# Kernel optimization log

Hardware: AMD Instinct MI355X
Metric: run time of the kernel (lower is better)

Reference implementation:

```python
import jax, jax.numpy as jnp
import numpy as np

# SLAYER SRM-ALPHA neuron / simulation constants (from netParams)
THETA = 10.0      # spike threshold
TAU_SR = 10.0     # PSP (SRM) time constant
TAU_REF = 1.0     # refractory time constant
SCALE_REF = 2.0
TAU_RHO = 1.0     # surrogate-gradient width (unused in fwd)
SCALE_RHO = 1.0
TS = 1.0
K_SRM = 100       # truncation of alpha kernel (values < 1e-4 beyond this)
K_REF = 16

def _alpha_kernel(tau, K, mult):
    t = jnp.arange(K, dtype=jnp.float32) * TS
    return mult * (t / tau) * jnp.exp(1.0 - t / tau)

SRM_KERNEL = _alpha_kernel(TAU_SR, K_SRM, 1.0)                       # eps(t)
REF_KERNEL = _alpha_kernel(TAU_REF, K_REF, -2.0 * THETA * SCALE_REF)  # nu(t)

def heaviside(u):
    return (u >= THETA).astype(u.dtype)

def psp(x):
    # causal temporal convolution with SRM alpha kernel; x: (..., T)
    T = x.shape[-1]
    K = SRM_KERNEL.shape[0]
    flat = x.reshape(-1, 1, T)  # (N, C=1, T)
    out = jax.lax.conv_general_dilated(flat, SRM_KERNEL[::-1].reshape(1, 1, K),
                                       (1,), [(K - 1, 0)])
    return out.reshape(x.shape)

def spike(v):
    # SLAYER spike generation with refractory feedback; v: (..., T)
    refk = REF_KERNEL[1:]          # refractory affects strictly future steps
    L = refk.shape[0]
    vT = jnp.moveaxis(v, -1, 0)    # (T, ...)
    pend0 = jnp.zeros(vT.shape[1:] + (L,), v.dtype)  # pending refractory contributions
    def step(pend, vt):
        u = vt + pend[..., 0]
        s = heaviside(u)
        pend = jnp.concatenate([pend[..., 1:], jnp.zeros_like(pend[..., :1])], axis=-1) \
               + s[..., None] * refk
        return pend, s
    _, sT = jax.lax.scan(step, pend0, vT)
    return jnp.moveaxis(sT, 0, -1)

def conv_t(x, W, pad):
    # per-timestep 2D conv (slayer.conv uses Conv3d with kernel (k,k,1), no bias)
    B, C, H, Wd, T = x.shape
    xt = jnp.transpose(x, (0, 4, 1, 2, 3)).reshape(B * T, C, H, Wd)
    y = jax.lax.conv_general_dilated(xt, W, (1, 1), [(pad, pad), (pad, pad)])
    Co, Ho, Wo = y.shape[1:]
    return jnp.transpose(y.reshape(B, T, Co, Ho, Wo), (0, 2, 3, 4, 1))

def pool_t(x):
    # slayer.pool(2): 2x2 sum-pool with constant weight 1.1*theta per element
    s = jax.lax.reduce_window(x, 0.0, jax.lax.add, (1, 1, 2, 2, 1), (1, 1, 2, 2, 1), 'VALID')
    return s * (1.1 * THETA)

def _forward(spikeInput, W1, W2, W3, W4, Wfc):
    x = spike(conv_t(psp(spikeInput), W1, 1))   # (B,16,48,48,T)
    x = spike(pool_t(psp(x)))                   # (B,16,24,24,T)
    x = spike(conv_t(psp(x), W2, 1))            # (B,32,24,24,T)
    x = spike(pool_t(psp(x)))                   # (B,32,12,12,T)
    x = spike(conv_t(psp(x), W3, 1))            # (B,64,12,12,T)
    x = spike(pool_t(psp(x)))                   # (B,64,6,6,T)
    x = spike(conv_t(psp(x), W4, 1))            # (B,64,6,6,T)
    x = spike(jnp.einsum('bchwt,kchw->bkt', psp(x), Wfc))  # (B,10,T)
    return x

def setup_inputs():
    key = jax.random.key(0)
    ks = jax.random.split(key, 6)
    B, T = 4, 200
    spikeInput = (jax.random.uniform(ks[0], (B, 2, 50, 50, T)) < 0.05).astype(jnp.float32)
    W1 = 0.5 * jax.random.normal(ks[1], (16, 2, 5, 5), jnp.float32)
    W2 = 0.25 * jax.random.normal(ks[2], (32, 16, 3, 3), jnp.float32)
    W3 = 0.25 * jax.random.normal(ks[3], (64, 32, 3, 3), jnp.float32)
    W4 = 0.25 * jax.random.normal(ks[4], (64, 64, 3, 3), jnp.float32)
    Wfc = 0.1 * jax.random.normal(ks[5], (10, 64, 6, 6), jnp.float32)
    return {"spikeInput": spikeInput, "W1": W1, "W2": W2, "W3": W3, "W4": W4, "Wfc": Wfc}

def reference(spikeInput, W1, W2, W3, W4, Wfc):
    return _forward(spikeInput, W1, W2, W3, W4, Wfc)
```

## Files before the change

kernel.cpp:

```cpp
#include <hip/hip_runtime.h>
#include <math.h>


#define THETA 10.0f
#define RSTRIDE 204

__global__ void prep_kernel(const float* __restrict__ W1, const float* __restrict__ W2,
                            const float* __restrict__ W3, const float* __restrict__ W4,
                            float* HQ, float* rk,
                            float* wt1, float* wt2, float* wt3, float* wt4) {
    int i = blockIdx.x * 256 + threadIdx.x;
    if (i < 144) {
        int k = i - 15;
        float val = 0.0f;
        if (k >= 0 && k <= 99) {
            float tf = (float)k;
            float x = tf / 10.0f;
            val = x * (float)exp((double)(1.0f - x));
        }
        HQ[i] = val;
    } else if (i < 160) {
        int j = i - 144;
        if (j < 15) {
            float t = (float)(j + 1);
            rk[j] = (-40.0f * t) * (float)exp((double)(1.0f - t));
        }
    } else if (i < 960) {
        int j = i - 160, co = j / 50, tp = j % 50;
        wt1[tp * 16 + co] = W1[j];
    } else if (i < 5568) {
        int j = i - 960, co = j / 144, tp = j % 144;
        wt2[tp * 32 + co] = W2[j];
    } else if (i < 24000) {
        int j = i - 5568, co = j / 288, tp = j % 288;
        wt3[tp * 64 + co] = W3[j];
    } else if (i < 60864) {
        int j = i - 24000, co = j / 576, tp = j % 576;
        wt4[tp * 64 + co] = W4[j];
    }
}

#define FIR_STEP(A0, A1, A2, A3, qx, qy, qz, qw, hA, hB)  \
    A0 = fmaf(hA.x, qw, A0);                              \
    A1 = fmaf(hA.y, qw, A1);                              \
    A2 = fmaf(hA.z, qw, A2);                              \
    A3 = fmaf(hA.w, qw, A3);                              \
    A0 = fmaf(hA.y, qz, A0);                              \
    A1 = fmaf(hA.z, qz, A1);                              \
    A2 = fmaf(hA.w, qz, A2);                              \
    A3 = fmaf(hB.x, qz, A3);                              \
    A0 = fmaf(hA.z, qy, A0);                              \
    A1 = fmaf(hA.w, qy, A1);                              \
    A2 = fmaf(hB.x, qy, A2);                              \
    A3 = fmaf(hB.y, qy, A3);                              \
    A0 = fmaf(hA.w, qx, A0);                              \
    A1 = fmaf(hB.x, qx, A1);                              \
    A2 = fmaf(hB.y, qx, A2);                              \
    A3 = fmaf(hB.z, qx, A3);

#define SCAN4(XV, p, rk)                                          \
    {                                                             \
        float u_, sv_;                                            \
        u_ = XV.x + p[0]; sv_ = (u_ >= THETA) ? 1.0f : 0.0f;      \
        XV.x = sv_;                                               \
        _Pragma("unroll")                                         \
        for (int i_ = 0; i_ < 14; ++i_) p[i_] = fmaf(sv_, rk[i_], p[i_ + 1]); \
        p[14] = sv_ * rk[14];                                     \
        u_ = XV.y + p[0]; sv_ = (u_ >= THETA) ? 1.0f : 0.0f;      \
        XV.y = sv_;                                               \
        _Pragma("unroll")                                         \
        for (int i_ = 0; i_ < 14; ++i_) p[i_] = fmaf(sv_, rk[i_], p[i_ + 1]); \
        p[14] = sv_ * rk[14];                                     \
        u_ = XV.z + p[0]; sv_ = (u_ >= THETA) ? 1.0f : 0.0f;      \
        XV.z = sv_;                                               \
        _Pragma("unroll")                                         \
        for (int i_ = 0; i_ < 14; ++i_) p[i_] = fmaf(sv_, rk[i_], p[i_ + 1]); \
        p[14] = sv_ * rk[14];                                     \
        u_ = XV.w + p[0]; sv_ = (u_ >= THETA) ? 1.0f : 0.0f;      \
        XV.w = sv_;                                               \
        _Pragma("unroll")                                         \
        for (int i_ = 0; i_ < 14; ++i_) p[i_] = fmaf(sv_, rk[i_], p[i_ + 1]); \
        p[14] = sv_ * rk[14];                                     \
    }

__device__ __forceinline__ void fir_run2(const float* __restrict__ row,
                                         const float4* __restrict__ HQ4,
                                         int t0, int jend, float4 (&acc)[2]) {
    float4 A = HQ4[2], B = HQ4[3], C = HQ4[4];
    const float* bp = row + t0 + 4;
    for (int j = 0; j <= jend; ++j) {
        const float4 qv = *reinterpret_cast<const float4*>(bp);
        const float4 N = HQ4[j + 5];
        FIR_STEP(acc[0].x, acc[0].y, acc[0].z, acc[0].w,
                 qv.x, qv.y, qv.z, qv.w, A, B)
        FIR_STEP(acc[1].x, acc[1].y, acc[1].z, acc[1].w,
                 qv.x, qv.y, qv.z, qv.w, B, C)
        A = B; B = C; C = N;
        bp -= 4;
    }
}

__device__ static const signed char FIR_ITEMS8[8][4] = {
    {24, 12, 8, -1}, {22, 21, 4, -1}, {20, 19, 3, -1}, {18, 17, 2, -1},
    {16, 15, 1, 0},  {13, 11, 5, -1}, {14, 10, 6, -1}, {23, 9, 7, -1}};

template <bool SCAN>
__global__ __launch_bounds__(512) void spikepsp_kernel(const float* __restrict__ in,
                                                       float* __restrict__ out,
                                                       const float* __restrict__ HQ,
                                                       const float* __restrict__ rkt,
                                                       int n) {
    __shared__ __align__(16) float tile[64 * RSTRIDE];
    const int l = threadIdx.x & 63;
    const int w = threadIdx.x >> 6;
    const int s0 = blockIdx.x * 64;
    for (int i = threadIdx.x; i < 3200; i += 512) {
        const int slot = i / 50, q = i - slot * 50;
        const int ser = s0 + slot;
        float4 v = make_float4(0.f, 0.f, 0.f, 0.f);
        if (ser < n) v = *reinterpret_cast<const float4*>(in + (long)ser * 200 + 4 * q);
        *reinterpret_cast<float4*>(&tile[slot * RSTRIDE + 4 * q]) = v;
    }
    __syncthreads();
    if (SCAN) {
        if (w == 0) {
            float rk[15];
            #pragma unroll
            for (int i = 0; i < 15; ++i) rk[i] = rkt[i];
            float p[15];
            #pragma unroll
            for (int i = 0; i < 15; ++i) p[i] = 0.0f;
            float* row = tile + l * RSTRIDE;
            for (int tq = 0; tq < 50; ++tq) {
                float4 xv = *reinterpret_cast<const float4*>(&row[4 * tq]);
                SCAN4(xv, p, rk)
                *reinterpret_cast<float4*>(&row[4 * tq]) = xv;
            }
        }
        __syncthreads();
    }
    const bool valid = (s0 + l) < n;
    const float* row = tile + l * RSTRIDE;
    const float4* HQ4 = reinterpret_cast<const float4*>(HQ);
    float* op = out + (long)(s0 + l) * 200;
    #pragma unroll
    for (int k = 0; k < 4; ++k) {
        const int id = FIR_ITEMS8[w][k];
        if (id < 0) break;
        const int t0 = 8 * id;
        const int jend = ((2 * id < 25) ? 2 * id : 25) + 1;
        float4 acc[2];
        acc[0] = make_float4(0.f, 0.f, 0.f, 0.f);
        acc[1] = make_float4(0.f, 0.f, 0.f, 0.f);
        fir_run2(row, HQ4, t0, jend, acc);
        if (valid) {
            *reinterpret_cast<float4*>(op + t0) = acc[0];
            *reinterpret_cast<float4*>(op + t0 + 4) = acc[1];
        }
    }
}

__global__ __launch_bounds__(512) void spikepsppool_kernel(const float* __restrict__ in,
                                                           float* __restrict__ out,
                                                           const float* __restrict__ HQ,
                                                           const float* __restrict__ rkt,
                                                           int C, int HO, int WO) {
    __shared__ __align__(16) float tile[64 * RSTRIDE];
    __shared__ int sbase[64];
    const int l = threadIdx.x & 63;
    const int w = threadIdx.x >> 6;
    const int o0 = blockIdx.x * 16;
    const int H = 2 * HO, W = 2 * WO;
    if (threadIdx.x < 64) {
        const int oi = threadIdx.x >> 2, p = threadIdx.x & 3;
        const int o = o0 + oi;
        const int wo = o % WO; int tmp = o / WO;
        const int ho = tmp % HO; tmp /= HO;
        const int c = tmp % C; const int b = tmp / C;
        sbase[threadIdx.x] = ((b * C + c) * H + 2 * ho + (p >> 1)) * W + 2 * wo + (p & 1);
    }
    __syncthreads();
    for (int i = threadIdx.x; i < 3200; i += 512) {
        const int slot = i / 50, q = i - slot * 50;
        const float4 v = *reinterpret_cast<const float4*>(in + (long)sbase[slot] * 200 + 4 * q);
        *reinterpret_cast<float4*>(&tile[slot * RSTRIDE + 4 * q]) = v;
    }
    __syncthreads();
    if (w == 0) {
        float rk[15];
        #pragma unroll
        for (int i = 0; i < 15; ++i) rk[i] = rkt[i];
        float p[15];
        #pragma unroll
        for (int i = 0; i < 15; ++i) p[i] = 0.0f;
        float* row = tile + l * RSTRIDE;
        for (int tq = 0; tq < 50; ++tq) {
            float4 xv = *reinterpret_cast<const float4*>(&row[4 * tq]);
            SCAN4(xv, p, rk)
            *reinterpret_cast<float4*>(&row[4 * tq]) = xv;
        }
    }
    __syncthreads();
    const int qb = l & ~3;
    const float* row = tile + l * RSTRIDE;
    const float4* HQ4 = reinterpret_cast<const float4*>(HQ);
    float* op = out + (long)(o0 + (l >> 2)) * 200;
    auto qsum = [&](float v) -> float {
        const float v0 = __shfl(v, qb + 0);
        const float v1 = __shfl(v, qb + 1);
        const float v2 = __shfl(v, qb + 2);
        const float v3 = __shfl(v, qb + 3);
        return (((v0 + v1) + v2) + v3) * 11.0f;
    };
    #pragma unroll
    for (int k = 0; k < 4; ++k) {
        const int id = FIR_ITEMS8[w][k];
        if (id < 0) break;
        const int t0 = 8 * id;
        const int jend = ((2 * id < 25) ? 2 * id : 25) + 1;
        float4 acc[2];
        acc[0] = make_float4(0.f, 0.f, 0.f, 0.f);
        acc[1] = make_float4(0.f, 0.f, 0.f, 0.f);
        fir_run2(row, HQ4, t0, jend, acc);
        #pragma unroll
        for (int d = 0; d < 2; ++d) {
            float4 r;
            r.x = qsum(acc[d].x); r.y = qsum(acc[d].y);
            r.z = qsum(acc[d].z); r.w = qsum(acc[d].w);
            if ((l & 3) == 0)
                *reinterpret_cast<float4*>(op + t0 + 4 * d) = r;
        }
    }
}

template <int K, int PAD, int CI, int COG>
__global__ __launch_bounds__(256) void conv_kernel(const float* __restrict__ x,
                                                   const float* __restrict__ wt,
                                                   float* __restrict__ out,
                                                   int Co, int H, int W,
                                                   int HO, int WO) {
    const int l = threadIdx.x & 63;
    const int wv = threadIdx.x >> 6;
    if (l >= 50) return;
    const int p = blockIdx.x * 4 + wv;
    const int wo = p % WO, ho = p / WO;
    const int co0 = blockIdx.y * COG;
    const int b = blockIdx.z;
    const int t0 = l * 4;
    float4 acc[COG];
    #pragma unroll
    for (int c = 0; c < COG; ++c) acc[c] = make_float4(0.f, 0.f, 0.f, 0.f);
    const float* xb = x + ((long)b * CI * H * W) * 200 + t0;
    for (int ci = 0; ci < CI; ++ci) {
        #pragma unroll
        for (int kh = 0; kh < K; ++kh) {
            const int hi = ho + kh - PAD;
            if (hi < 0 || hi >= H) continue;
            #pragma unroll
            for (int kw = 0; kw < K; ++kw) {
                const int wi = wo + kw - PAD;
                if (wi < 0 || wi >= W) continue;
                const float4 v = *reinterpret_cast<const float4*>(
                    xb + ((long)(ci * H + hi) * W + wi) * 200);
                const float* wp = wt + ((ci * K + kh) * K + kw) * Co + co0;
                #pragma unroll
                for (int c = 0; c < COG; ++c) {
                    const float wv_ = wp[c];
                    acc[c].x = fmaf(wv_, v.x, acc[c].x);
                    acc[c].y = fmaf(wv_, v.y, acc[c].y);
                    acc[c].z = fmaf(wv_, v.z, acc[c].z);
                    acc[c].w = fmaf(wv_, v.w, acc[c].w);
                }
            }
        }
    }
    const long hwN = (long)HO * WO;
    const long ob = ((long)(b * Co + co0) * HO + ho) * WO + wo;
    #pragma unroll
    for (int c = 0; c < COG; ++c)
        *reinterpret_cast<float4*>(out + (ob + c * hwN) * 200 + t0) = acc[c];
}

template <int CI, int COG>
__global__ __launch_bounds__(256) void conv3_kernel(const float* __restrict__ x,
                                                    const float* __restrict__ wt,
                                                    float* __restrict__ out,
                                                    int Co, int H, int W) {
    const int l = threadIdx.x & 63;
    const int wv = threadIdx.x >> 6;
    if (l >= 50) return;
    const int p = blockIdx.x * 4 + wv;
    const int wo = p % W, ho = p / W;
    const int co0 = blockIdx.y * COG;
    const int b = blockIdx.z;
    const int t0 = l * 4;
    float4 acc[COG];
    #pragma unroll
    for (int c = 0; c < COG; ++c) acc[c] = make_float4(0.f, 0.f, 0.f, 0.f);

    bool vm[9];
    #pragma unroll
    for (int i = 0; i < 9; ++i) {
        const int hi = ho + i / 3 - 1, wi = wo + i % 3 - 1;
        vm[i] = (hi >= 0) && (hi < H) && (wi >= 0) && (wi < W);
    }
    const long cis = (long)H * W * 200;
    const float* pb = x + (long)b * CI * cis + ((long)(ho - 1) * W + (wo - 1)) * 200 + t0;

    float4 bufA[9], bufB[9];
    auto ld = [&](int ci, float4 (&B)[9]) {
        const float* pc = pb + ci * cis;
        #pragma unroll
        for (int i = 0; i < 9; ++i) {
            B[i] = vm[i] ? *reinterpret_cast<const float4*>(pc + ((i / 3) * W + (i % 3)) * 200)
                         : make_float4(0.f, 0.f, 0.f, 0.f);
        }
    };
    auto fm = [&](const float4 (&B)[9], int ci) {
        #pragma unroll
        for (int i = 0; i < 9; ++i) {
            const float* wp = wt + (ci * 9 + i) * Co + co0;
            #pragma unroll
            for (int c = 0; c < COG; ++c) {
                const float wv_ = wp[c];
                acc[c].x = fmaf(wv_, B[i].x, acc[c].x);
                acc[c].y = fmaf(wv_, B[i].y, acc[c].y);
                acc[c].z = fmaf(wv_, B[i].z, acc[c].z);
                acc[c].w = fmaf(wv_, B[i].w, acc[c].w);
            }
        }
    };

    ld(0, bufA);
    #pragma unroll 1
    for (int ci = 0; ci < CI; ci += 2) {
        ld(ci + 1, bufB);
        fm(bufA, ci);
        if (ci + 2 < CI) ld(ci + 2, bufA);
        fm(bufB, ci + 1);
    }

    const long hwN = (long)H * W;
    const long ob = ((long)(b * Co + co0) * H + ho) * W + wo;
    #pragma unroll
    for (int c = 0; c < COG; ++c)
        *reinterpret_cast<float4*>(out + (ob + c * hwN) * 200 + t0) = acc[c];
}

__global__ __launch_bounds__(256) void spike_kernel(const float* __restrict__ v,
                                                    float* __restrict__ s,
                                                    const float* __restrict__ rkt,
                                                    int n) {
    const int nid = blockIdx.x * 256 + threadIdx.x;
    if (nid >= n) return;
    float rk[15];
    #pragma unroll
    for (int i = 0; i < 15; ++i) rk[i] = rkt[i];
    float p[15];
    #pragma unroll
    for (int i = 0; i < 15; ++i) p[i] = 0.0f;
    const float* vp = v + (long)nid * 200;
    float* sp = s + (long)nid * 200;
    for (int t = 0; t < 200; ++t) {
        const float u = vp[t] + p[0];
        const float sv = (u >= THETA) ? 1.0f : 0.0f;
        sp[t] = sv;
        #pragma unroll
        for (int i = 0; i < 14; ++i) p[i] = fmaf(sv, rk[i], p[i + 1]);
        p[14] = sv * rk[14];
    }
}

__global__ __launch_bounds__(256) void fc_kernel(const float* __restrict__ x,
                                                 const float* __restrict__ wf,
                                                 float* __restrict__ out) {
    __shared__ __align__(16) float xs[8 * 2308];
    const int b = blockIdx.x;
    const int t0 = blockIdx.y * 8;
    const int tid = threadIdx.x;
    const float* xb = x + (long)b * 2304 * 200 + t0;
    for (int i = tid; i < 4608; i += 256) {
        const int m = i >> 1, qh = (i & 1) * 4;
        const float4 v = *reinterpret_cast<const float4*>(xb + (long)m * 200 + qh);
        xs[(qh + 0) * 2308 + m] = v.x;
        xs[(qh + 1) * 2308 + m] = v.y;
        xs[(qh + 2) * 2308 + m] = v.z;
        xs[(qh + 3) * 2308 + m] = v.w;
    }
    __syncthreads();
    if (tid < 80) {
        const int k = tid >> 3, q = tid & 7;
        float a = 0.0f;
        const float* wp = wf + k * 2304;
        const float* xp = xs + q * 2308;
        for (int m4 = 0; m4 < 2304; m4 += 4) {
            const float4 xv = *reinterpret_cast<const float4*>(xp + m4);
            const float4 wv = *reinterpret_cast<const float4*>(wp + m4);
            a = fmaf(wv.x, xv.x, a);
            a = fmaf(wv.y, xv.y, a);
            a = fmaf(wv.z, xv.z, a);
            a = fmaf(wv.w, xv.w, a);
        }
        out[((long)b * 10 + k) * 200 + t0 + q] = a;
    }
}

extern "C" void kernel_launch(void* const* d_in, const int* in_sizes, int n_in,
                              void* d_out, int out_size, void* d_ws, size_t ws_size,
                              hipStream_t stream) {
    const float* x_in = (const float*)d_in[0];
    const float* W1 = (const float*)d_in[1];
    const float* W2 = (const float*)d_in[2];
    const float* W3 = (const float*)d_in[3];
    const float* W4 = (const float*)d_in[4];
    const float* Wfc = (const float*)d_in[5];
    float* outp = (float*)d_out;

    float* ws = (float*)d_ws;
    float* HQ  = ws;
    float* rk  = ws + 144;
    float* wt1 = ws + 160;
    float* wt2 = wt1 + 800;
    float* wt3 = wt2 + 4608;
    float* wt4 = wt3 + 18432;
    float* A   = wt4 + 36864;
    float* B   = A + 7372800;
    float* C   = B + 29491200;

    hipLaunchKernelGGL(prep_kernel, dim3(238), dim3(256), 0, stream,
                       W1, W2, W3, W4, HQ, rk, wt1, wt2, wt3, wt4);

    hipLaunchKernelGGL((spikepsp_kernel<false>), dim3(313), dim3(512), 0, stream,
                       x_in, A, HQ, rk, 20000);
    hipLaunchKernelGGL((conv_kernel<5, 1, 2, 16>), dim3(2304 / 4, 1, 4), dim3(256), 0, stream,
                       A, wt1, B, 16, 50, 50, 48, 48);
    hipLaunchKernelGGL(spikepsppool_kernel, dim3(36864 / 16), dim3(512), 0, stream,
                       B, A, HQ, rk, 16, 24, 24);
    hipLaunchKernelGGL((spikepsp_kernel<true>), dim3(36864 / 64), dim3(512), 0, stream,
                       A, B, HQ, rk, 36864);
    hipLaunchKernelGGL((conv3_kernel<16, 8>), dim3(576 / 4, 4, 4), dim3(256), 0, stream,
                       B, wt2, C, 32, 24, 24);
    hipLaunchKernelGGL(spikepsppool_kernel, dim3(18432 / 16), dim3(512), 0, stream,
                       C, A, HQ, rk, 32, 12, 12);
    hipLaunchKernelGGL((spikepsp_kernel<true>), dim3(18432 / 64), dim3(512), 0, stream,
                       A, B, HQ, rk, 18432);
    hipLaunchKernelGGL((conv3_kernel<32, 8>), dim3(144 / 4, 8, 4), dim3(256), 0, stream,
                       B, wt3, C, 64, 12, 12);
    hipLaunchKernelGGL(spikepsppool_kernel, dim3(9216 / 16), dim3(512), 0, stream,
                       C, A, HQ, rk, 64, 6, 6);
    hipLaunchKernelGGL((spikepsp_kernel<true>), dim3(9216 / 64), dim3(512), 0, stream,
                       A, B, HQ, rk, 9216);
    hipLaunchKernelGGL((conv3_kernel<64, 4>), dim3(36 / 4, 16, 4), dim3(256), 0, stream,
                       B, wt4, C, 64, 6, 6);
    hipLaunchKernelGGL((spikepsp_kernel<true>), dim3(9216 / 64), dim3(512), 0, stream,
                       C, B, HQ, rk, 9216);
    hipLaunchKernelGGL(fc_kernel, dim3(4, 25), dim3(256), 0, stream, B, Wfc, A);
    hipLaunchKernelGGL(spike_kernel, dim3(1), dim3(256), 0, stream, A, outp, rk, 40);
    (void)in_sizes; (void)n_in; (void)out_size; (void)ws_size;
}
```

Baseline: 676.9 us.

## Overlap spike scan tail with PSP FIR on early timesteps

The spike scan is split into two phases: timesteps 0-127 first, then 128-199. While wave 0 finishes the scan on the later timesteps, the other seven waves compute FIR outputs for the first 128 timesteps, which only depend on already-scanned inputs. A final phase spreads the remaining output chunks across all waves using a new single-float4 FIR helper. This targets the serial scan, during which seven of eight waves sat idle, at the cost of an extra barrier and a less even work split.

```diff
diff --git a/kernel.cpp b/kernel.cpp
--- a/kernel.cpp
+++ b/kernel.cpp
@@ -100,9 +100,33 @@
     }
 }
 
+__device__ __forceinline__ void fir_half(const float* __restrict__ row,
+                                         const float4* __restrict__ HQ4,
+                                         int s0, float4& acc) {
+    const int cc = s0 >> 2;
+    const int jmax = ((cc - 1 < 25) ? cc - 1 : 25) + 1;
+    float4 A = HQ4[3], B = HQ4[4];
+    const float* bp = row + s0;
+    for (int j = 0; j <= jmax; ++j) {
+        const float4 qv = *reinterpret_cast<const float4*>(bp);
+        const float4 N = HQ4[j + 5];
+        FIR_STEP(acc.x, acc.y, acc.z, acc.w, qv.x, qv.y, qv.z, qv.w, A, B)
+        A = B; B = N;
+        bp -= 4;
+    }
+}
+
 __device__ static const signed char FIR_ITEMS8[8][4] = {
     {24, 12, 8, -1}, {22, 21, 4, -1}, {20, 19, 3, -1}, {18, 17, 2, -1},
     {16, 15, 1, 0},  {13, 11, 5, -1}, {14, 10, 6, -1}, {23, 9, 7, -1}};
+
+__device__ static const signed char FIR_B[7][3] = {
+    {15, 4, -1}, {14, 3, 0}, {13, 5, -1}, {12, 6, -1},
+    {11, 7, -1}, {10, 8, -1}, {9, 2, 1}};
+
+__device__ static const signed char FIR_C[8][3] = {
+    {32, 33, -1}, {34, 35, -1}, {36, 37, -1}, {38, 39, -1},
+    {40, 41, -1}, {42, 43, -1}, {44, 45, 46}, {47, 48, 49}};
 
 template <bool SCAN>
 __global__ __launch_bounds__(512) void spikepsp_kernel(const float* __restrict__ in,
@@ -113,49 +137,85 @@
     __shared__ __align__(16) float tile[64 * RSTRIDE];
     const int l = threadIdx.x & 63;
     const int w = threadIdx.x >> 6;
-    const int s0 = blockIdx.x * 64;
+    const int s0b = blockIdx.x * 64;
     for (int i = threadIdx.x; i < 3200; i += 512) {
         const int slot = i / 50, q = i - slot * 50;
-        const int ser = s0 + slot;
+        const int ser = s0b + slot;
         float4 v = make_float4(0.f, 0.f, 0.f, 0.f);
         if (ser < n) v = *reinterpret_cast<const float4*>(in + (long)ser * 200 + 4 * q);
         *reinterpret_cast<float4*>(&tile[slot * RSTRIDE + 4 * q]) = v;
     }
     __syncthreads();
+    const bool valid = (s0b + l) < n;
+    const float* row = tile + l * RSTRIDE;
+    const float4* HQ4 = reinterpret_cast<const float4*>(HQ);
+    float* op = out + (long)(s0b + l) * 200;
     if (SCAN) {
+        float rk[15];
+        float p[15];
         if (w == 0) {
-            float rk[15];
             #pragma unroll
             for (int i = 0; i < 15; ++i) rk[i] = rkt[i];
-            float p[15];
             #pragma unroll
             for (int i = 0; i < 15; ++i) p[i] = 0.0f;
-            float* row = tile + l * RSTRIDE;
-            for (int tq = 0; tq < 50; ++tq) {
-                float4 xv = *reinterpret_cast<const float4*>(&row[4 * tq]);
+            float* srow = tile + l * RSTRIDE;
+            for (int tq = 0; tq < 32; ++tq) {
+                float4 xv = *reinterpret_cast<const float4*>(&srow[4 * tq]);
                 SCAN4(xv, p, rk)
-                *reinterpret_cast<float4*>(&row[4 * tq]) = xv;
+                *reinterpret_cast<float4*>(&srow[4 * tq]) = xv;
             }
         }
         __syncthreads();
-    }
-    const bool valid = (s0 + l) < n;
-    const float* row = tile + l * RSTRIDE;
-    const float4* HQ4 = reinterpret_cast<const float4*>(HQ);
-    float* op = out + (long)(s0 + l) * 200;
-    #pragma unroll
-    for (int k = 0; k < 4; ++k) {
-        const int id = FIR_ITEMS8[w][k];
-        if (id < 0) break;
-        const int t0 = 8 * id;
-        const int jend = ((2 * id < 25) ? 2 * id : 25) + 1;
-        float4 acc[2];
-        acc[0] = make_float4(0.f, 0.f, 0.f, 0.f);
-        acc[1] = make_float4(0.f, 0.f, 0.f, 0.f);
-        fir_run2(row, HQ4, t0, jend, acc);
-        if (valid) {
-            *reinterpret_cast<float4*>(op + t0) = acc[0];
-            *reinterpret_cast<float4*>(op + t0 + 4) = acc[1];
+        if (w == 0) {
+            float* srow = tile + l * RSTRIDE;
+            for (int tq = 32; tq < 50; ++tq) {
+                float4 xv = *reinterpret_cast<const float4*>(&srow[4 * tq]);
+                SCAN4(xv, p, rk)
+                *reinterpret_cast<float4*>(&srow[4 * tq]) = xv;
+            }
+        } else {
+            #pragma unroll
+            for (int k = 0; k < 3; ++k) {
+                const int id = FIR_B[w - 1][k];
+                if (id < 0) break;
+                const int t0 = 8 * id;
+                const int jend = ((2 * id < 25) ? 2 * id : 25) + 1;
+                float4 acc[2];
+                acc[0] = make_float4(0.f, 0.f, 0.f, 0.f);
+                acc[1] = make_float4(0.f, 0.f, 0.f, 0.f);
+                fir_run2(row, HQ4, t0, jend, acc);
+                if (valid) {
+                    *reinterpret_cast<float4*>(op + t0) = acc[0];
+                    *reinterpret_cast<float4*>(op + t0 + 4) = acc[1];
+                }
+            }
+        }
+        __syncthreads();
+        #pragma unroll
+        for (int k = 0; k < 3; ++k) {
+            const int cc = FIR_C[w][k];
+            if (cc < 0) break;
+            const int s0 = 4 * cc;
+            float4 acc = make_float4(0.f, 0.f, 0.f, 0.f);
+            fir_half(row, HQ4, s0, acc);
+            if (valid)
+                *reinterpret_cast<float4*>(op + s0) = acc;
+        }
+    } else {
+        #pragma unroll
+        for (int k = 0; k < 4; ++k) {
+            const int id = FIR_ITEMS8[w][k];
+            if (id < 0) break;
+            const int t0 = 8 * id;
+            const int jend = ((2 * id < 25) ? 2 * id : 25) + 1;
+            float4 acc[2];
+            acc[0] = make_float4(0.f, 0.f, 0.f, 0.f);
+            acc[1] = make_float4(0.f, 0.f, 0.f, 0.f);
+            fir_run2(row, HQ4, t0, jend, acc);
+            if (valid) {
+                *reinterpret_cast<float4*>(op + t0) = acc[0];
+                *reinterpret_cast<float4*>(op + t0 + 4) = acc[1];
+            }
         }
     }
 }
@@ -172,33 +232,18 @@
     const int o0 = blockIdx.x * 16;
     const int H = 2 * HO, W = 2 * WO;
     if (threadIdx.x < 64) {
-        const int oi = threadIdx.x >> 2, p = threadIdx.x & 3;
+        const int oi = threadIdx.x >> 2, pp = threadIdx.x & 3;
         const int o = o0 + oi;
         const int wo = o % WO; int tmp = o / WO;
         const int ho = tmp % HO; tmp /= HO;
         const int c = tmp % C; const int b = tmp / C;
-        sbase[threadIdx.x] = ((b * C + c) * H + 2 * ho + (p >> 1)) * W + 2 * wo + (p & 1);
+        sbase[threadIdx.x] = ((b * C + c) * H + 2 * ho + (pp >> 1)) * W + 2 * wo + (pp & 1);
     }
     __syncthreads();
     for (int i = threadIdx.x; i < 3200; i += 512) {
         const int slot = i / 50, q = i - slot * 50;
         const float4 v = *reinterpret_cast<const float4*>(in + (long)sbase[slot] * 200 + 4 * q);
         *reinterpret_cast<float4*>(&tile[slot * RSTRIDE + 4 * q]) = v;
-    }
-    __syncthreads();
-    if (w == 0) {
-        float rk[15];
-        #pragma unroll
-        for (int i = 0; i < 15; ++i) rk[i] = rkt[i];
-        float p[15];
-        #pragma unroll
-        for (int i = 0; i < 15; ++i) p[i] = 0.0f;
-        float* row = tile + l * RSTRIDE;
-        for (int tq = 0; tq < 50; ++tq) {
-            float4 xv = *reinterpret_cast<const float4*>(&row[4 * tq]);
-            SCAN4(xv, p, rk)
-            *reinterpret_cast<float4*>(&row[4 * tq]) = xv;
-        }
     }
     __syncthreads();
     const int qb = l & ~3;
@@ -212,24 +257,62 @@
         const float v3 = __shfl(v, qb + 3);
         return (((v0 + v1) + v2) + v3) * 11.0f;
     };
-    #pragma unroll
-    for (int k = 0; k < 4; ++k) {
-        const int id = FIR_ITEMS8[w][k];
-        if (id < 0) break;
-        const int t0 = 8 * id;
-        const int jend = ((2 * id < 25) ? 2 * id : 25) + 1;
-        float4 acc[2];
-        acc[0] = make_float4(0.f, 0.f, 0.f, 0.f);
-        acc[1] = make_float4(0.f, 0.f, 0.f, 0.f);
-        fir_run2(row, HQ4, t0, jend, acc);
-        #pragma unroll
-        for (int d = 0; d < 2; ++d) {
-            float4 r;
-            r.x = qsum(acc[d].x); r.y = qsum(acc[d].y);
-            r.z = qsum(acc[d].z); r.w = qsum(acc[d].w);
-            if ((l & 3) == 0)
-                *reinterpret_cast<float4*>(op + t0 + 4 * d) = r;
-        }
+    float rk[15];
+    float p[15];
+    if (w == 0) {
+        #pragma unroll
+        for (int i = 0; i < 15; ++i) rk[i] = rkt[i];
+        #pragma unroll
+        for (int i = 0; i < 15; ++i) p[i] = 0.0f;
+        float* srow = tile + l * RSTRIDE;
+        for (int tq = 0; tq < 32; ++tq) {
+            float4 xv = *reinterpret_cast<const float4*>(&srow[4 * tq]);
+            SCAN4(xv, p, rk)
+            *reinterpret_cast<float4*>(&srow[4 * tq]) = xv;
+        }
+    }
+    __syncthreads();
+    if (w == 0) {
+        float* srow = tile + l * RSTRIDE;
+        for (int tq = 32; tq < 50; ++tq) {
+            float4 xv = *reinterpret_cast<const float4*>(&srow[4 * tq]);
+            SCAN4(xv, p, rk)
+            *reinterpret_cast<float4*>(&srow[4 * tq]) = xv;
+        }
+    } else {
+        #pragma unroll
+        for (int k = 0; k < 3; ++k) {
+            const int id = FIR_B[w - 1][k];
+            if (id < 0) break;
+            const int t0 = 8 * id;
+            const int jend = ((2 * id < 25) ? 2 * id : 25) + 1;
+            float4 acc[2];
+            acc[0] = make_float4(0.f, 0.f, 0.f, 0.f);
+            acc[1] = make_float4(0.f, 0.f, 0.f, 0.f);
+            fir_run2(row, HQ4, t0, jend, acc);
+            #pragma unroll
+            for (int d = 0; d < 2; ++d) {
+                float4 r;
+                r.x = qsum(acc[d].x); r.y = qsum(acc[d].y);
+                r.z = qsum(acc[d].z); r.w = qsum(acc[d].w);
+                if ((l & 3) == 0)
+                    *reinterpret_cast<float4*>(op + t0 + 4 * d) = r;
+            }
+        }
+    }
+    __syncthreads();
+    #pragma unroll
+    for (int k = 0; k < 3; ++k) {
+        const int cc = FIR_C[w][k];
+        if (cc < 0) break;
+        const int s0 = 4 * cc;
+        float4 acc = make_float4(0.f, 0.f, 0.f, 0.f);
+        fir_half(row, HQ4, s0, acc);
+        float4 r;
+        r.x = qsum(acc.x); r.y = qsum(acc.y);
+        r.z = qsum(acc.z); r.w = qsum(acc.w);
+        if ((l & 3) == 0)
+            *reinterpret_cast<float4*>(op + s0) = r;
     }
 }
 
```

Result: slower. 718.0 us (+6.1%).
